# Kernel optimization log

Hardware: AMD Instinct MI355X
Metric: run time of the kernel (lower is better)

Reference implementation:

```python
import jax, jax.numpy as jnp
import numpy as np

B, L_PROG = 8, 12
NUM_CLASSES, NUM_ATTRS = 256, 256
MAX_CONCEPTS, MAX_OBJECTS = 4096, 128
N_ATTR_PER_OBJ = 8
E, A, H = 64, 64, 256  # embed_dim, attention_dim, hidden_dim


def setup_inputs() -> dict:
    key = jax.random.key(0)
    ks = jax.random.split(key, 22)
    f = lambda k, shape: jax.random.normal(k, shape, dtype=jnp.float32) * 0.05
    return {
        'class_embIn': f(ks[0], (NUM_CLASSES, E)),
        'class_embOut': f(ks[1], (NUM_CLASSES, E)),
        'attr_embIn': f(ks[2], (NUM_ATTRS, E)),
        'attr_embOut': f(ks[3], (NUM_ATTRS, E)),
        'concept_embIn': f(ks[4], (MAX_CONCEPTS, E)),
        'concept_embOut': f(ks[5], (MAX_CONCEPTS, E)),
        'meta_init': f(ks[6], (A,)),
        'object_init': f(ks[7], (E,)),
        'attention_init': f(ks[8], (A,)),
        'axon_w1': f(ks[9], (A + E, H)), 'axon_b1': f(ks[10], (H,)),
        'axon_w2': f(ks[11], (H, E)), 'axon_b2': f(ks[12], (E,)),
        'meta_w1': f(ks[13], (E + A, H)), 'meta_b1': f(ks[14], (H,)),
        'meta_w2': f(ks[15], (H, A)), 'meta_b2': f(ks[16], (A,)),
        'program_ops': jax.random.randint(ks[17], (B, L_PROG), 0, 3),
        'program_args': jax.random.randint(ks[18], (B, L_PROG), 0, MAX_CONCEPTS),
        'gt_classes': jax.random.randint(ks[19], (B, MAX_OBJECTS), 0, NUM_CLASSES),
        'gt_attributes': jax.random.randint(ks[20], (B, MAX_OBJECTS, N_ATTR_PER_OBJ), 0, NUM_ATTRS),
    }


def _mlp(x, w1, b1, w2, b2):
    return jnp.maximum(x @ w1 + b1, 0.0) @ w2 + b2


def reference(class_embIn, class_embOut, attr_embIn, attr_embOut,
              concept_embIn, concept_embOut, meta_init, object_init,
              attention_init, axon_w1, axon_b1, axon_w2, axon_b2,
              meta_w1, meta_b1, meta_w2, meta_b2,
              program_ops, program_args, gt_classes, gt_attributes):
    Bb, Lp = program_ops.shape
    C = concept_embIn.shape[0]
    N = C + gt_classes.shape[1]  # dim_concept = max_concepts + max_objects

    # object embeddings: class embedding + sum of attribute embeddings  (B, O, E)
    objIn = class_embIn[gt_classes] + attr_embIn[gt_attributes].sum(axis=2)
    objOut = class_embOut[gt_classes] + attr_embOut[gt_attributes].sum(axis=2)

    # thought = [concepts ; objects]  (B, N, E)
    thoughtIn = jnp.concatenate(
        [jnp.broadcast_to(concept_embIn[None], (Bb, C, E)), objIn], axis=1)
    thoughtOut = jnp.concatenate(
        [jnp.broadcast_to(concept_embOut[None], (Bb, C, E)), objOut], axis=1)

    args_emb = concept_embOut[program_args]          # (B, L, E)
    is_mode = (program_ops == 0).astype(jnp.float32)     # (B, L)
    is_insert = (program_ops == 1).astype(jnp.float32)
    is_transfer = (program_ops == 2).astype(jnp.float32)

    meta0 = jnp.broadcast_to(meta_init[None], (Bb, A))
    att0 = jnp.broadcast_to(attention_init[None, None], (Bb, N, A))

    def step(carry, xs):
        meta, attention = carry
        m, ins, tr, arg = xs  # (B,), (B,), (B,), (B,E)
        new_meta = _mlp(jnp.concatenate([meta, arg], axis=-1),
                        meta_w1, meta_b1, meta_w2, meta_b2)
        meta = m[:, None] * new_meta + (1.0 - m[:, None]) * meta
        # insert: meta scaled by mean_e(arg * thoughtOut)
        proj = (arg[:, None, :] * thoughtOut).mean(axis=-1)        # (B, N)
        att_insert = meta[:, None, :] * proj[:, :, None]           # (B, N, A)
        # transfer: bilinear scores thoughtIn . axon, mean-aggregate attention
        mb = jnp.broadcast_to(meta[:, None, :], (Bb, N, A))
        axon = _mlp(jnp.concatenate([thoughtOut, mb], axis=-1),
                    axon_w1, axon_b1, axon_w2, axon_b2)            # (B, N, E)
        scores = jnp.einsum('bje,bke->bjk', thoughtIn, axon)       # (B, N, N)
        att_transfer = jnp.einsum('bjk,bka->bja', scores, attention) / N
        attention = attention + ins[:, None, None] * att_insert \
                              + tr[:, None, None] * att_transfer
        return (meta, attention), None

    xs = (is_mode.T, is_insert.T, is_transfer.T,
          jnp.transpose(args_emb, (1, 0, 2)))
    (meta, attention), _ = jax.lax.scan(step, (meta0, att0), xs)

    output_length = jnp.mean(attention ** 2, axis=-1)              # (B, N)
    return jax.nn.log_softmax(output_length, axis=1)
```

## Files before the change

### kernel.cpp

```cpp
#include <hip/hip_runtime.h>
#include <hip/hip_bf16.h>

typedef __hip_bfloat16 bf16;
typedef float f32x4 __attribute__((ext_vector_type(4)));
typedef short s16x8 __attribute__((ext_vector_type(8)));

#define B_    8
#define LP    12
#define NC    4096
#define NO    128
#define NAPO  8
#define NN    4224
#define E_    64
#define A_    64
#define H_    256
#define QC    80
#define PROJ0 65
#define NCHUNK 17

#define TOT_IN 688896
#define QTF_C  67584
#define QTF_B  337920
#define TB_P   983040

struct Ptr16 { const void* p[16]; };
union U8 { s16x8 v; unsigned u[4]; };

__device__ __forceinline__ float b2f(bf16 x){ return __bfloat162float(x); }
__device__ __forceinline__ float bs2f(unsigned short s){
  union { unsigned u; float f; } x; x.u = ((unsigned)s) << 16; return x.f;
}
__device__ __forceinline__ unsigned short f2bs(float f){
  bf16 h = __float2bfloat16(f);
  union { bf16 h; unsigned short s; } x; x.h = h; return x.s;
}
__device__ __forceinline__ unsigned pack2(float a, float b){
  return (unsigned)f2bs(a) | ((unsigned)f2bs(b) << 16);
}
__device__ __forceinline__ float lo16f(unsigned w){
  union { unsigned u; float f; } x; x.u = w << 16; return x.f;
}
__device__ __forceinline__ float hi16f(unsigned w){
  union { unsigned u; float f; } x; x.u = w & 0xffff0000u; return x.f;
}
__device__ __forceinline__ float rdval(const void* p, int i, int fl){
  return fl ? ((const float*)p)[i] : bs2f(((const unsigned short*)p)[i]);
}

__global__ void k_prep(Ptr16 ps, int* flag, float* dst,
                       unsigned short* awFrag,
                       const int* gtc, const int* gta,
                       float* objIn, float* objOut, float* qsum_esum){
  int tid = threadIdx.x;
  const unsigned short* u = (const unsigned short*)ps.p[4];
  int hit = (((u[tid*16] >> 7) & 0xFF) >= 137) ? 1 : 0;
  unsigned long long m = __ballot(hit);
  int fl = (m != 0ULL) ? 1 : 0;
  int mb = blockIdx.x;
  if (mb < 673){
    int idx = (mb*256 + tid)*4;
    if (idx >= TOT_IN) return;
    constexpr int cum[17] = {0,16384,32768,49152,65536,327680,589824,589888,589952,
                             622720,622976,639360,639424,672192,672448,688832,688896};
    int t = 0;
    #pragma unroll
    for (int i=1;i<16;i++) if (idx >= cum[i]) t = i;
    int off = idx - cum[t];
    float4 v;
    if (fl){
      v = *(const float4*)((const float*)ps.p[t] + off);
    } else {
      uint2 sv = *(const uint2*)((const unsigned short*)ps.p[t] + off);
      v.x = lo16f(sv.x); v.y = hi16f(sv.x);
      v.z = lo16f(sv.y); v.w = hi16f(sv.y);
    }
    *(float4*)(dst + idx) = v;
  } else if (mb < 737){
    int idx = (mb-673)*256 + tid;
    int j = idx & 7;
    int lane = (idx >> 3) & 63;
    int mm = (idx >> 9) & 15;
    int kc = idx >> 13;
    int e = kc*32 + (lane>>4)*8 + j;
    int h = mm*16 + (lane&15);
    awFrag[idx] = f2bs(rdval(ps.p[8], e*H_ + h, fl));
  } else if (mb < 993){
    int idx = (mb-737)*256 + tid;
    int e = idx & 63; int bo = idx >> 6;
    int cls = gtc[bo];
    float vi = rdval(ps.p[0], cls*E_ + e, fl);
    float vo = rdval(ps.p[1], cls*E_ + e, fl);
    const int* ga = gta + bo*NAPO;
    #pragma unroll
    for (int j=0;j<NAPO;j++){
      int at = ga[j];
      vi += rdval(ps.p[2], at*E_ + e, fl);
      vo += rdval(ps.p[3], at*E_ + e, fl);
    }
    objIn[idx] = vi; objOut[idx] = vo;
  } else {
    if (tid < 656) qsum_esum[tid] = 0.f;
    if (tid == 0) *flag = fl;
  }
}

__device__ __forceinline__ void mid_meta(char* smem, int b,
                       const float* conceptOut, const float* meta_init,
                       const float* mw1, const float* mb1, const float* mw2, const float* mb2,
                       const float* aw1, const float* ab1,
                       const int* ops, const int* args,
                       float* metaAll, float* metaH){
  unsigned* mw1p = (unsigned*)smem;
  unsigned* mw2p = (unsigned*)(smem + 65536);
  unsigned* aw1p = (unsigned*)(smem + 98304);
  float* meta_s  = (float*)(smem + 131072);
  float* argx    = (float*)(smem + 131328);
  float* hid     = (float*)(smem + 131584);
  float* part    = (float*)(smem + 132608);
  int tid = threadIdx.x;

  for (int i=tid; i<64*256; i+=256){
    int j2 = i >> 8, t = i & 255;
    mw1p[i] = pack2(mw1[(2*j2)*H_ + t], mw1[(2*j2+1)*H_ + t]);
  }
  for (int i=tid; i<128*64; i+=256){
    int h2 = i >> 6, a = i & 63;
    mw2p[i] = pack2(mw2[(2*h2)*A_ + a], mw2[(2*h2+1)*A_ + a]);
  }
  for (int i=tid; i<32*256; i+=256){
    int a2 = i >> 8, t = i & 255;
    aw1p[i] = pack2(aw1[(E_+2*a2)*H_ + t], aw1[(E_+2*a2+1)*H_ + t]);
  }
  float r_mb1 = mb1[tid];
  float r_ab1 = ab1[tid];
  float r_mb2 = (tid < A_) ? mb2[tid] : 0.f;
  if (tid < A_) meta_s[tid] = meta_init[tid];
  __syncthreads();

  float mh = r_ab1;
  for (int a2=0;a2<32;a2++){
    unsigned w = aw1p[a2*256 + tid];
    float2 mp = *(const float2*)&meta_s[2*a2];
    mh = fmaf(mp.x, lo16f(w), mh);
    mh = fmaf(mp.y, hi16f(w), mh);
  }

  for (int t=0;t<LP;t++){
    int op  = ops[b*LP + t];
    if (op == 0){
      int arg = args[b*LP + t];
      if (tid >= 64 && tid < 128) argx[tid-64] = conceptOut[arg*E_ + (tid-64)];
      __syncthreads();
      float acc = r_mb1;
      for (int j2=0;j2<32;j2++){
        unsigned w = mw1p[j2*256 + tid];
        float2 xp = *(const float2*)&meta_s[2*j2];
        acc = fmaf(xp.x, lo16f(w), acc);
        acc = fmaf(xp.y, hi16f(w), acc);
      }
      for (int j2=0;j2<32;j2++){
        unsigned w = mw1p[(32+j2)*256 + tid];
        float2 xp = *(const float2*)&argx[2*j2];
        acc = fmaf(xp.x, lo16f(w), acc);
        acc = fmaf(xp.y, hi16f(w), acc);
      }
      hid[tid] = fmaxf(acc, 0.f);
      __syncthreads();
      int wv_ = tid >> 6, l = tid & 63;
      float acc2 = 0.f;
      for (int h2 = wv_*32; h2 < wv_*32+32; h2++){
        unsigned w = mw2p[h2*64 + l];
        float2 hp = *(const float2*)&hid[2*h2];
        acc2 = fmaf(hp.x, lo16f(w), acc2);
        acc2 = fmaf(hp.y, hi16f(w), acc2);
      }
      part[wv_*64 + l] = acc2;
      __syncthreads();
      if (tid < A_){
        float s = part[tid] + part[64+tid] + part[128+tid] + part[192+tid] + r_mb2;
        meta_s[tid] = s;
      }
      __syncthreads();
      mh = r_ab1;
      for (int a2=0;a2<32;a2++){
        unsigned w = aw1p[a2*256 + tid];
        float2 mp = *(const float2*)&meta_s[2*a2];
        mh = fmaf(mp.x, lo16f(w), mh);
        mh = fmaf(mp.y, hi16f(w), mh);
      }
    }
    if (tid < A_) metaAll[(b*LP+t)*A_ + tid] = meta_s[tid];
    metaH[(b*LP+t)*H_ + tid] = mh;
  }
}

__device__ __forceinline__ void mid_qt(char* smem, int idx,
                       const float* conceptIn, const float* conceptOut, const int* args,
                       const float* objIn, const float* objOut,
                       unsigned short* QTf, float* qsum){
  float* tile = (float*)smem;
  float* argv = (float*)(smem + 66560);
  float* qs   = (float*)(smem + 69632);
  int b = idx / NCHUNK, chunk = idx % NCHUNK;
  int tid = threadIdx.x;
  int rows = (chunk < 16) ? 256 : 128;
  int n0 = chunk*256;
  int n = n0 + tid;
  bool valid = (tid < rows);
  if (tid < 80) qs[tid] = 0.f;
  unsigned short* Qb = QTf + (size_t)b*QTF_B + ((n>>5)*512 + (n&31));
  {
    const float* src = (chunk < 16) ? (conceptIn + (size_t)n0*E_) : (objIn + (size_t)b*NO*E_);
    int tot = rows*64;
    for (int i=tid; i<tot; i+=256) tile[(i>>6)*65 + (i&63)] = src[i];
  }
  __syncthreads();
  if (valid){
    Qb[0] = 0x3F80;
    Qb[4*QTF_C + 13*32] = 0;
    Qb[4*QTF_C + 14*32] = 0;
    Qb[4*QTF_C + 15*32] = 0;
    for (int e=0;e<64;e++){
      int qc = 1+e;
      Qb[(qc>>4)*QTF_C + (qc&15)*32] = f2bs(tile[tid*65 + e]);
    }
    for (int i=0;i<64;i++){
      int e = (i + tid) & 63;
      atomicAdd(&qs[1+e], tile[tid*65+e]);
    }
  }
  __syncthreads();
  for (int i=tid;i<LP*E_;i+=256) argv[i] = conceptOut[args[b*LP + (i>>6)]*E_ + (i&63)];
  {
    const float* src = (chunk < 16) ? (conceptOut + (size_t)n0*E_) : (objOut + (size_t)b*NO*E_);
    int tot = rows*64;
    for (int i=tid; i<tot; i+=256) tile[(i>>6)*65 + (i&63)] = src[i];
  }
  __syncthreads();
  float dots[LP];
  #pragma unroll
  for (int t=0;t<LP;t++) dots[t] = 0.f;
  for (int e=0;e<64;e++){
    float o = tile[tid*65 + e];
    #pragma unroll
    for (int t=0;t<LP;t++) dots[t] += o*argv[t*64+e];
  }
  #pragma unroll
  for (int t=0;t<LP;t++){
    float v = valid ? dots[t]*(1.f/E_) : 0.f;
    if (valid){
      int qc = PROJ0+t;
      Qb[(qc>>4)*QTF_C + (qc&15)*32] = f2bs(v);
    }
    float r = v;
    #pragma unroll
    for (int off=32; off>0; off>>=1) r += __shfl_down(r, off, 64);
    if ((tid & 63) == 0) atomicAdd(&qs[PROJ0+t], r);
  }
  __syncthreads();
  if (tid < 80) atomicAdd(&qsum[b*QC + tid], qs[tid]);
  if (chunk == 0 && tid == 0) atomicAdd(&qsum[b*QC], (float)NN);
}

__device__ __forceinline__ void mid_base(int blk,
                       const float* conceptOut, const float* objOut,
                       const unsigned short* awFrag,
                       unsigned short* AoptC, unsigned short* AoptO){
  int n0 = blk * 64;
  int tid = threadIdx.x;
  int w = tid >> 6, l = tid & 63, quad = l >> 4, lq = l & 15;
  int n = n0 + w*16 + lq;
  const float* src = (n < NC) ? (conceptOut + (size_t)n*E_) : (objOut + (size_t)(n-NC)*E_);
  f32x4 acc[16];
  #pragma unroll
  for (int m=0;m<16;m++) acc[m] = (f32x4){0.f,0.f,0.f,0.f};
  #pragma unroll
  for (int kc=0;kc<2;kc++){
    s16x8 bfr;
    #pragma unroll
    for (int j=0;j<8;j++) bfr[j] = (short)f2bs(src[kc*32 + quad*8 + j]);
    const unsigned short* ap = awFrag + ((size_t)(kc*16)*64 + l)*8;
    #pragma unroll
    for (int m=0;m<16;m++){
      s16x8 af = *(const s16x8*)(ap + (size_t)m*64*8);
      acc[m] = __builtin_amdgcn_mfma_f32_16x16x32_bf16(af, bfr, acc[m], 0, 0, 0);
    }
  }
  int nl = n & 31;
  if (n < NC){
    int nch = n >> 5;
    #pragma unroll
    for (int m=0;m<16;m++){
      #pragma unroll
      for (int r=0;r<4;r++)
        AoptC[(size_t)(m*128 + nch)*512 + (quad*4+r)*32 + nl] = f2bs(acc[m][r]);
    }
  } else {
    int no = n - NC; int bb = no >> 7; int oc = (no & 127) >> 5;
    #pragma unroll
    for (int m=0;m<16;m++){
      #pragma unroll
      for (int r=0;r<4;r++)
        AoptO[(size_t)((bb*16 + m)*4 + oc)*512 + (quad*4+r)*32 + nl] = f2bs(acc[m][r]);
    }
  }
}

__global__ __launch_bounds__(256) void k_mid(
    const float* conceptIn, const float* conceptOut,
    const float* meta_init, const float* mw1, const float* mb1, const float* mw2, const float* mb2,
    const float* aw1, const float* ab1, const int* ops, const int* args,
    const float* objIn, const float* objOut, const unsigned short* awFrag,
    float* metaAll, float* metaH, unsigned short* QTf, float* qsum,
    unsigned short* AoptC, unsigned short* AoptO){
  __shared__ __align__(16) char smem[133888];
  int mb = blockIdx.x;
  if (mb < 8)
    mid_meta(smem, mb, conceptOut, meta_init, mw1, mb1, mw2, mb2, aw1, ab1, ops, args, metaAll, metaH);
  else if (mb < 144)
    mid_qt(smem, mb-8, conceptIn, conceptOut, args, objIn, objOut, QTf, qsum);
  else
    mid_base(mb-144, conceptOut, objOut, awFrag, AoptC, AoptO);
}

__global__ __launch_bounds__(64) void k_T(const unsigned short* AoptC, const unsigned short* AoptO,
                                          const unsigned short* QTf, const float* metaH,
                                          const int* ops, unsigned* TB){
  int bid = blockIdx.x;
  int kh = bid & 7; int ht = (bid >> 3) & 3; int bt = bid >> 5; int b = bt / LP;
  if (ops[bt] != 2) return;
  int l = threadIdx.x, quad = l >> 4, lq = l & 15;
  int off = lq*32 + quad*8;
  int start = (kh < 4) ? (kh*17) : (68 + (kh-4)*16);
  int count = (kh < 4) ? 17 : 16;
  float mh[4];
  #pragma unroll
  for (int s=0;s<4;s++) mh[s] = metaH[(size_t)bt*H_ + ht*64 + s*16 + lq];
  f32x4 acc[4][5];
  #pragma unroll
  for (int s=0;s<4;s++){
    #pragma unroll
    for (int c=0;c<5;c++) acc[s][c] = (f32x4){0.f,0.f,0.f,0.f};
  }
  const unsigned short* QTb = QTf + (size_t)b*QTF_B + off;
  const unsigned short* AC  = AoptC + (size_t)(ht*4)*65536 + off;
  const unsigned short* AO  = AoptO + (size_t)(b*16 + ht*4)*2048 + off;
  for (int it=0; it<count; it++){
    int nchunk = start + it;
    U8 bfr[5];
    #pragma unroll
    for (int c=0;c<5;c++)
      bfr[c].v = *(const s16x8*)(QTb + (size_t)c*QTF_C + (size_t)nchunk*512);
    bool isC = (nchunk < 128);
    #pragma unroll
    for (int s=0;s<4;s++){
      U8 a;
      a.v = isC ? *(const s16x8*)(AC + (size_t)s*65536 + (size_t)nchunk*512)
                : *(const s16x8*)(AO + (size_t)s*2048 + (size_t)(nchunk-128)*512);
      float mhs = mh[s];
      U8 af;
      #pragma unroll
      for (int d=0;d<4;d++){
        unsigned wv = a.u[d];
        float lo = fmaxf(__uint_as_float(wv << 16) + mhs, 0.f);
        float hi = fmaxf(__uint_as_float(wv & 0xffff0000u) + mhs, 0.f);
        af.u[d] = __builtin_amdgcn_perm(__float_as_uint(hi), __float_as_uint(lo), 0x07060302u);
      }
      #pragma unroll
      for (int c=0;c<5;c++)
        acc[s][c] = __builtin_amdgcn_mfma_f32_16x16x32_bf16(af.v, bfr[c].v, acc[s][c], 0, 0, 0);
    }
  }
  unsigned* Tp = TB + (size_t)kh*TB_P + ((size_t)bt*4 + ht)*2560;
  #pragma unroll
  for (int s=0;s<4;s++){
    #pragma unroll
    for (int c=0;c<5;c++){
      uint2 v;
      v.x = pack2(acc[s][c][0], acc[s][c][1]);
      v.y = pack2(acc[s][c][2], acc[s][c][3]);
      *(uint2*)(Tp + (s*5+c)*128 + l*2) = v;
    }
  }
}

__global__ __launch_bounds__(256) void k_U(const unsigned* TB,
                                           const float* w2, const float* b2v,
                                           const float* qsum, const int* ops,
                                           float* Ut0, float* Ut1){
  __shared__ float Wt[128*64];
  __shared__ float Tt[128*81];
  int bid = blockIdx.x;
  int kq = bid & 1; int bt = bid >> 1; int b = bt / LP;
  if (ops[bt] != 2) return;
  int tid = threadIdx.x;
  for (int i=tid; i<8192; i+=256){
    int hl = i >> 6, e = i & 63;
    Wt[i] = w2[(kq*128 + hl)*E_ + e];
  }
  #pragma unroll
  for (int half=0; half<2; half++){
    const unsigned* base = TB + ((size_t)bt*4 + kq*2 + half)*2560;
    for (int i2=tid; i2<2560; i2+=256){
      float lo = 0.f, hi = 0.f;
      #pragma unroll
      for (int p=0;p<8;p++){
        unsigned w = base[(size_t)p*TB_P + i2];
        lo += lo16f(w); hi += hi16f(w);
      }
      int idx = 2*i2;
      int sc = idx >> 8; int ll = (idx >> 2) & 63; int r = idx & 3;
      int s = sc/5, c = sc - s*5;
      int hl = half*64 + s*16 + ((ll>>4)<<2) + r;
      int qc = c*16 + (ll&15);
      Tt[hl*81 + qc]     = lo;
      Tt[(hl+1)*81 + qc] = hi;
    }
  }
  __syncthreads();
  int el = tid & 15, ql = tid >> 4;
  float acc[4][5];
  #pragma unroll
  for (int i=0;i<4;i++){
    #pragma unroll
    for (int j=0;j<5;j++) acc[i][j]=0.f;
  }
  #pragma unroll 4
  for (int kk=0; kk<128; kk++){
    float4 wv = *(const float4*)&Wt[kk*64 + el*4];
    float ww[4] = {wv.x, wv.y, wv.z, wv.w};
    const float* tp = &Tt[kk*81 + ql*5];
    #pragma unroll
    for (int j=0;j<5;j++){
      float tv = tp[j];
      #pragma unroll
      for (int i=0;i<4;i++) acc[i][j] = fmaf(ww[i], tv, acc[i][j]);
    }
  }
  const float invN = 1.f/NN;
  float* Up = (kq ? Ut1 : Ut0) + (size_t)bt*5120;
  if (kq == 0){
    float be[4], qv[5];
    #pragma unroll
    for (int i=0;i<4;i++) be[i] = b2v[el*4+i];
    #pragma unroll
    for (int j=0;j<5;j++) qv[j] = qsum[b*QC + ql*5+j];
    #pragma unroll
    for (int i=0;i<4;i++){
      #pragma unroll
      for (int j=0;j<5;j++)
        Up[(el*4+i)*QC + ql*5+j] = (acc[i][j] + be[i]*qv[j]) * invN;
    }
  } else {
    #pragma unroll
    for (int i=0;i<4;i++){
      #pragma unroll
      for (int j=0;j<5;j++)
        Up[(el*4+i)*QC + ql*5+j] = acc[i][j] * invN;
    }
  }
}

__global__ __launch_bounds__(256) void k_rec(const float* Ut0, const float* Ut1, const float* metaAll,
                                             const int* ops, const float* att_init, float* Cm){
  __shared__ float C[QC*65];
  __shared__ float Ul[2][64*81];
  int b = blockIdx.x, tid = threadIdx.x;
  int w = tid >> 6, l = tid & 63, quad = l >> 4, lq = l & 15;
  for (int i=tid;i<QC*65;i+=256) C[i] = 0.f;
  if (tid < A_) C[tid] = att_init[tid];
  {
    const float* U0 = Ut0 + (size_t)(b*LP)*5120;
    const float* U1 = Ut1 + (size_t)(b*LP)*5120;
    #pragma unroll
    for (int k=0;k<5;k++){
      int i = tid*4 + k*1024;
      float4 v0 = *(const float4*)&U0[i];
      float4 v1 = *(const float4*)&U1[i];
      int r = i/80, c = i%80;
      Ul[0][r*81+c]   = v0.x+v1.x; Ul[0][r*81+c+1] = v0.y+v1.y;
      Ul[0][r*81+c+2] = v0.z+v1.z; Ul[0][r*81+c+3] = v0.w+v1.w;
    }
  }
  __syncthreads();
  for (int t=0;t<LP;t++){
    float4 rv0[5], rv1[5];
    if (t < LP-1){
      const float* U0 = Ut0 + (size_t)(b*LP+t+1)*5120;
      const float* U1 = Ut1 + (size_t)(b*LP+t+1)*5120;
      #pragma unroll
      for (int k=0;k<5;k++){
        rv0[k] = *(const float4*)&U0[tid*4 + k*1024];
        rv1[k] = *(const float4*)&U1[tid*4 + k*1024];
      }
    }
    int op = ops[b*LP + t];
    f32x4 acc[4];
    if (op == 2){
      const float* Uc = Ul[t&1];
      U8 af[3][4];
      #pragma unroll
      for (int k0t=0;k0t<3;k0t++){
        #pragma unroll
        for (int s=0;s<4;s++){
          int e = s*16 + lq;
          int qb = k0t*32 + quad*8;
          float v[8];
          #pragma unroll
          for (int j=0;j<8;j++){
            int qc = qb + j;
            v[j] = (qc < QC) ? Uc[e*81 + qc] : 0.f;
          }
          #pragma unroll
          for (int d=0;d<4;d++) af[k0t][s].u[d] = pack2(v[2*d], v[2*d+1]);
        }
      }
      U8 bf[3];
      #pragma unroll
      for (int k0t=0;k0t<3;k0t++){
        int kb = k0t*32 + quad*8;
        float v[8];
        #pragma unroll
        for (int j=0;j<8;j++){
          int k = kb + j;
          v[j] = (k < QC) ? C[k*65 + w*16 + lq] : 0.f;
        }
        #pragma unroll
        for (int d=0;d<4;d++) bf[k0t].u[d] = pack2(v[2*d], v[2*d+1]);
      }
      #pragma unroll
      for (int s=0;s<4;s++){
        acc[s] = (f32x4){0.f,0.f,0.f,0.f};
        #pragma unroll
        for (int k0t=0;k0t<3;k0t++)
          acc[s] = __builtin_amdgcn_mfma_f32_16x16x32_bf16(af[k0t][s].v, bf[k0t].v, acc[s], 0, 0, 0);
      }
    }
    __syncthreads();
    if (op == 2){
      #pragma unroll
      for (int s=0;s<4;s++){
        #pragma unroll
        for (int r=0;r<4;r++){
          int e = s*16 + quad*4 + r;
          C[(1+e)*65 + w*16 + lq] += acc[s][r];
        }
      }
    } else if (op == 1){
      if (tid < A_) C[(PROJ0+t)*65 + tid] += metaAll[(b*LP+t)*A_ + tid];
    }
    if (t < LP-1){
      float* Un = Ul[(t+1)&1];
      #pragma unroll
      for (int k=0;k<5;k++){
        int i = tid*4 + k*1024;
        int r = i/80, c = i%80;
        Un[r*81+c]   = rv0[k].x+rv1[k].x; Un[r*81+c+1] = rv0[k].y+rv1[k].y;
        Un[r*81+c+2] = rv0[k].z+rv1[k].z; Un[r*81+c+3] = rv0[k].w+rv1[k].w;
      }
    }
    __syncthreads();
  }
  for (int i=tid;i<QC*A_;i+=256) Cm[b*QC*A_ + i] = C[(i>>6)*65 + (i&63)];
}

__global__ __launch_bounds__(128) void k_out(const unsigned short* QTf, const float* Cm,
                                             float* ol, float* esum){
  __shared__ float C[QC*A_];
  __shared__ float wsum[2];
  int b = blockIdx.x / 33, rem = blockIdx.x % 33;
  int tid = threadIdx.x;
  for (int i=tid;i<QC*A_;i+=128) C[i] = Cm[b*QC*A_ + i];
  __syncthreads();
  int n = rem*128 + tid;
  float y[A_];
  #pragma unroll
  for (int a=0;a<A_;a++) y[a]=0.f;
  const unsigned short* Qb = QTf + (size_t)b*QTF_B + ((n>>5)*512 + (n&31));
  for (int j=0;j<QC;j++){
    float qvv = bs2f(Qb[(j>>4)*QTF_C + (j&15)*32]);
    const float* Cj = &C[j*A_];
    #pragma unroll
    for (int a=0;a<A_;a++) y[a] = fmaf(qvv, Cj[a], y[a]);
  }
  float s = 0.f;
  #pragma unroll
  for (int a=0;a<A_;a++) s = fmaf(y[a], y[a], s);
  float o = s * (1.f/A_);
  ol[(size_t)b*NN + n] = o;
  float contrib = expf(o);
  #pragma unroll
  for (int off=32; off>0; off>>=1) contrib += __shfl_down(contrib, off, 64);
  if ((tid & 63) == 0) wsum[tid>>6] = contrib;
  __syncthreads();
  if (tid == 0) atomicAdd(&esum[b], wsum[0]+wsum[1]);
}

__global__ void k_fin(const float* ol, const float* esum, const int* flag, void* out){
  int idx = blockIdx.x*256 + threadIdx.x;
  if (idx < B_*NN){
    int b = idx / NN;
    float v = ol[idx] - logf(esum[b]);
    if (*flag) ((float*)out)[idx] = v;
    else       ((bf16*)out)[idx]  = __float2bfloat16(v);
  }
}

extern "C" void kernel_launch(void* const* d_in, const int* in_sizes, int n_in,
                              void* d_out, int out_size, void* d_ws, size_t ws_size,
                              hipStream_t stream) {
  (void)in_sizes; (void)n_in; (void)out_size; (void)ws_size;
  const int* ops  = (const int*)d_in[17];
  const int* args = (const int*)d_in[18];
  const int* gtc  = (const int*)d_in[19];
  const int* gta  = (const int*)d_in[20];

  float* ws = (float*)d_ws;
  int* flag = (int*)ws;
  float* W  = ws + 16;

  const float* conceptIn  = W + 65536;
  const float* conceptOut = W + 327680;
  const float* meta_init  = W + 589824;
  const float* att_init   = W + 589888;
  const float* aw1        = W + 589952;
  const float* ab1        = W + 622720;
  const float* aw2        = W + 622976;
  const float* ab2        = W + 639360;
  const float* mw1        = W + 639424;
  const float* mb1        = W + 672192;
  const float* mw2        = W + 672448;
  const float* mb2        = W + 688832;

  constexpr size_t OFF_OBJIN   = 16 + TOT_IN;
  constexpr size_t OFF_OBJOUT  = OFF_OBJIN  + 65536;
  constexpr size_t OFF_METAALL = OFF_OBJOUT + 65536;
  constexpr size_t OFF_METAH   = OFF_METAALL + 6144;
  constexpr size_t OFF_QSUM    = OFF_METAH  + 24576;
  constexpr size_t OFF_ESUM    = OFF_QSUM   + 640;
  constexpr size_t OFF_UT0     = OFF_ESUM   + 16;
  constexpr size_t OFF_UT1     = OFF_UT0    + 491520;
  constexpr size_t OFF_CM      = OFF_UT1    + 491520;
  constexpr size_t OFF_OL      = OFF_CM     + 40960;
  constexpr size_t OFF_QTF     = OFF_OL     + 33792;
  constexpr size_t OFF_AOPTC   = OFF_QTF    + 1351680;
  constexpr size_t OFF_AOPTO   = OFF_AOPTC  + 524288;
  constexpr size_t OFF_AWF     = OFF_AOPTO  + 131072;
  constexpr size_t OFF_TB      = OFF_AWF    + 8192;

  float* objIn   = ws + OFF_OBJIN;
  float* objOut  = ws + OFF_OBJOUT;
  float* metaAll = ws + OFF_METAALL;
  float* metaH   = ws + OFF_METAH;
  float* qsum    = ws + OFF_QSUM;
  float* esum    = ws + OFF_ESUM;
  float* Ut0     = ws + OFF_UT0;
  float* Ut1     = ws + OFF_UT1;
  float* Cm      = ws + OFF_CM;
  float* ol      = ws + OFF_OL;
  unsigned short* QTf    = (unsigned short*)(ws + OFF_QTF);
  unsigned short* AoptC  = (unsigned short*)(ws + OFF_AOPTC);
  unsigned short* AoptO  = (unsigned short*)(ws + OFF_AOPTO);
  unsigned short* awFrag = (unsigned short*)(ws + OFF_AWF);
  unsigned* TB           = (unsigned*)(ws + OFF_TB);

  Ptr16 ps;
  const int src_idx[16] = {0,1,2,3,4,5,6,8,9,10,11,12,13,14,15,16};
  for (int i=0;i<16;i++) ps.p[i] = d_in[src_idx[i]];

  k_prep<<<994, 256, 0, stream>>>(ps, flag, W, awFrag, gtc, gta, objIn, objOut, qsum);
  k_mid <<<224, 256, 0, stream>>>(conceptIn, conceptOut, meta_init, mw1, mb1, mw2, mb2,
                                  aw1, ab1, ops, args, objIn, objOut, awFrag,
                                  metaAll, metaH, QTf, qsum, AoptC, AoptO);
  k_T   <<<B_*LP*4*8, 64, 0, stream>>>(AoptC, AoptO, QTf, metaH, ops, TB);
  k_U   <<<B_*LP*2, 256, 0, stream>>>(TB, aw2, ab2, qsum, ops, Ut0, Ut1);
  k_rec <<<B_, 256, 0, stream>>>(Ut0, Ut1, metaAll, ops, att_init, Cm);
  k_out <<<B_*33, 128, 0, stream>>>(QTf, Cm, ol, esum);
  k_fin <<<(B_*NN + 255)/256, 256, 0, stream>>>(ol, esum, flag, d_out);
}
```

Measured before the change: 238.0 us.

## Rewrite output projection with bf16 MFMA and skip U loads for non-transfer steps

The final output kernel previously did a scalar FP32 80x64 matrix product per row with 64 accumulators per thread. It now packs the C matrix into bf16 B-fragments and runs 16x16x32 MFMA tiles, one 16-row tile per wave, with shuffle reductions for the squared norm. Separately, the recurrence kernel now loads and stages U tiles only when the next op is a transfer, which avoids global reads that are never used. The bf16 conversion of C lowers the precision of the output path.

```diff
diff --git a/kernel.cpp b/kernel.cpp
--- a/kernel.cpp
+++ b/kernel.cpp
@@ -469,7 +469,7 @@
   int w = tid >> 6, l = tid & 63, quad = l >> 4, lq = l & 15;
   for (int i=tid;i<QC*65;i+=256) C[i] = 0.f;
   if (tid < A_) C[tid] = att_init[tid];
-  {
+  if (ops[b*LP] == 2){
     const float* U0 = Ut0 + (size_t)(b*LP)*5120;
     const float* U1 = Ut1 + (size_t)(b*LP)*5120;
     #pragma unroll
@@ -484,8 +484,9 @@
   }
   __syncthreads();
   for (int t=0;t<LP;t++){
+    int opn = (t < LP-1) ? ops[b*LP + t + 1] : 0;
     float4 rv0[5], rv1[5];
-    if (t < LP-1){
+    if (opn == 2){
       const float* U0 = Ut0 + (size_t)(b*LP+t+1)*5120;
       const float* U1 = Ut1 + (size_t)(b*LP+t+1)*5120;
       #pragma unroll
@@ -549,7 +550,7 @@
     } else if (op == 1){
       if (tid < A_) C[(PROJ0+t)*65 + tid] += metaAll[(b*LP+t)*A_ + tid];
     }
-    if (t < LP-1){
+    if (opn == 2){
       float* Un = Ul[(t+1)&1];
       #pragma unroll
       for (int k=0;k<5;k++){
@@ -564,36 +565,72 @@
   for (int i=tid;i<QC*A_;i+=256) Cm[b*QC*A_ + i] = C[(i>>6)*65 + (i&63)];
 }
 
-__global__ __launch_bounds__(128) void k_out(const unsigned short* QTf, const float* Cm,
+__global__ __launch_bounds__(256) void k_out(const unsigned short* QTf, const float* Cm,
                                              float* ol, float* esum){
-  __shared__ float C[QC*A_];
-  __shared__ float wsum[2];
-  int b = blockIdx.x / 33, rem = blockIdx.x % 33;
+  __shared__ float Cpad[QC*65];
+  __shared__ float wsum[4];
+  int b = blockIdx.x / 66, rem = blockIdx.x % 66;
   int tid = threadIdx.x;
-  for (int i=tid;i<QC*A_;i+=128) C[i] = Cm[b*QC*A_ + i];
-  __syncthreads();
-  int n = rem*128 + tid;
-  float y[A_];
-  #pragma unroll
-  for (int a=0;a<A_;a++) y[a]=0.f;
-  const unsigned short* Qb = QTf + (size_t)b*QTF_B + ((n>>5)*512 + (n&31));
-  for (int j=0;j<QC;j++){
-    float qvv = bs2f(Qb[(j>>4)*QTF_C + (j&15)*32]);
-    const float* Cj = &C[j*A_];
-    #pragma unroll
-    for (int a=0;a<A_;a++) y[a] = fmaf(qvv, Cj[a], y[a]);
-  }
-  float s = 0.f;
-  #pragma unroll
-  for (int a=0;a<A_;a++) s = fmaf(y[a], y[a], s);
-  float o = s * (1.f/A_);
-  ol[(size_t)b*NN + n] = o;
-  float contrib = expf(o);
-  #pragma unroll
-  for (int off=32; off>0; off>>=1) contrib += __shfl_down(contrib, off, 64);
-  if ((tid & 63) == 0) wsum[tid>>6] = contrib;
-  __syncthreads();
-  if (tid == 0) atomicAdd(&esum[b], wsum[0]+wsum[1]);
+  int w = tid >> 6, l = tid & 63, quad = l >> 4, lq = l & 15;
+  for (int i=tid; i<QC*A_; i+=256) Cpad[(i>>6)*65 + (i&63)] = Cm[b*QC*A_ + i];
+  __syncthreads();
+  U8 bfr[3][4];
+  #pragma unroll
+  for (int kk=0;kk<3;kk++){
+    #pragma unroll
+    for (int at=0;at<4;at++){
+      float v[8];
+      #pragma unroll
+      for (int jj=0;jj<8;jj++){
+        int j = kk*32 + quad*8 + jj;
+        v[jj] = (j < QC) ? Cpad[j*65 + at*16 + lq] : 0.f;
+      }
+      #pragma unroll
+      for (int d=0;d<4;d++) bfr[kk][at].u[d] = pack2(v[2*d], v[2*d+1]);
+    }
+  }
+  const unsigned short* Qb = QTf + (size_t)b*QTF_B;
+  int mt = rem*4 + w;
+  int nb = (mt>>1)*512 + (mt&1)*16 + lq;
+  f32x4 acc[4];
+  #pragma unroll
+  for (int at=0;at<4;at++) acc[at] = (f32x4){0.f,0.f,0.f,0.f};
+  #pragma unroll
+  for (int kk=0;kk<3;kk++){
+    U8 af;
+    #pragma unroll
+    for (int d=0;d<4;d++){
+      int j0 = kk*32 + quad*8 + 2*d;
+      int j1 = j0 + 1;
+      unsigned u0 = (j0 < QC) ? (unsigned)Qb[(j0>>4)*QTF_C + (j0&15)*32 + nb] : 0u;
+      unsigned u1 = (j1 < QC) ? (unsigned)Qb[(j1>>4)*QTF_C + (j1&15)*32 + nb] : 0u;
+      af.u[d] = u0 | (u1 << 16);
+    }
+    #pragma unroll
+    for (int at=0;at<4;at++)
+      acc[at] = __builtin_amdgcn_mfma_f32_16x16x32_bf16(af.v, bfr[kk][at].v, acc[at], 0, 0, 0);
+  }
+  float le = 0.f;
+  #pragma unroll
+  for (int r=0;r<4;r++){
+    float s = 0.f;
+    #pragma unroll
+    for (int at=0;at<4;at++) s = fmaf(acc[at][r], acc[at][r], s);
+    s += __shfl_xor(s, 1, 64);
+    s += __shfl_xor(s, 2, 64);
+    s += __shfl_xor(s, 4, 64);
+    s += __shfl_xor(s, 8, 64);
+    if (lq == 0){
+      float o = s * (1.f/A_);
+      ol[(size_t)b*NN + mt*16 + quad*4 + r] = o;
+      le += expf(o);
+    }
+  }
+  le += __shfl_down(le, 32, 64);
+  le += __shfl_down(le, 16, 64);
+  if (l == 0) wsum[w] = le;
+  __syncthreads();
+  if (tid == 0) atomicAdd(&esum[b], wsum[0]+wsum[1]+wsum[2]+wsum[3]);
 }
 
 __global__ void k_fin(const float* ol, const float* esum, const int* flag, void* out){
@@ -675,6 +712,6 @@
   k_T   <<<B_*LP*4*8, 64, 0, stream>>>(AoptC, AoptO, QTf, metaH, ops, TB);
   k_U   <<<B_*LP*2, 256, 0, stream>>>(TB, aw2, ab2, qsum, ops, Ut0, Ut1);
   k_rec <<<B_, 256, 0, stream>>>(Ut0, Ut1, metaAll, ops, att_init, Cm);
-  k_out <<<B_*33, 128, 0, stream>>>(QTf, Cm, ol, esum);
+  k_out <<<B_*66, 256, 0, stream>>>(QTf, Cm, ol, esum);
   k_fin <<<(B_*NN + 255)/256, 256, 0, stream>>>(ol, esum, flag, d_out);
 }
```

New measurement: 220.9 us. 7.2% less time.
